# Performance work log

Measured on AMD Instinct MI355X. Metric: run time of the kernel, lower is better.

Reference implementation:

```python
import jax, jax.numpy as jnp
import numpy as np

N_NODES = 1024
HID = 128
NODE_D = 133
BOND_D = 14
E_HALF = 8192  # directed edges; doubled with reverses -> 16384


def setup_inputs() -> dict:
    key = jax.random.key(0)
    ks = jax.random.split(key, 24)

    x = jax.random.normal(ks[0], (N_NODES, NODE_D), jnp.float32)
    edge_attr = jax.random.normal(ks[1], (2 * E_HALF, BOND_D), jnp.float32)
    src = jax.random.randint(ks[2], (E_HALF,), 0, N_NODES)
    dst = jax.random.randint(ks[3], (E_HALF,), 0, N_NODES)
    # bidirectional edges so every edge has a reverse (as _rev_edge_index assumes)
    edge_index = jnp.stack([jnp.concatenate([src, dst]), jnp.concatenate([dst, src])]).astype(jnp.int32)
    rev_edge_index = jnp.concatenate([jnp.arange(E_HALF) + E_HALF, jnp.arange(E_HALF)]).astype(jnp.int32)

    dissociable_masks = (jax.random.uniform(ks[4], (N_NODES,)) < 0.1).astype(jnp.int32)
    pka_raw = jax.random.uniform(ks[5], (N_NODES,), minval=0.0, maxval=14.0)
    valid = jax.random.uniform(ks[6], (N_NODES,)) < (1.0 / 16.0)
    pka_values = jnp.where(valid, pka_raw, jnp.nan).astype(jnp.float32)

    def lin(k, fi, fo):
        return (jax.random.normal(k, (fi, fo)) / np.sqrt(fi)).astype(jnp.float32)

    z = lambda n: jnp.zeros((n,), jnp.float32)
    inp = dict(x=x, edge_attr=edge_attr, pka_values=pka_values,
               dissociable_masks=dissociable_masks, edge_index=edge_index,
               rev_edge_index=rev_edge_index,
               Wi=lin(ks[7], NODE_D + BOND_D, HID), bi=z(HID),
               Wh=lin(ks[8], HID, HID), bh=z(HID),
               Wo=lin(ks[9], NODE_D + HID, HID), bo=z(HID),
               Wnt=lin(ks[10], NODE_D, HID), bnt=z(HID),
               Wc1=lin(ks[11], HID, 256), bc1=z(256),
               Wc2=lin(ks[12], 256, 64), bc2=z(64),
               Wc3=lin(ks[13], 64, 2), bc3=z(2),
               Wr1=lin(ks[14], HID, 256), br1=z(256),
               Wr2=lin(ks[15], 256, 64), br2=z(64),
               Wr3=lin(ks[16], 64, 1), br3=z(1),
               Wg=lin(ks[17], HID, HID), bg=z(HID))
    return inp


def reference(x, edge_attr, pka_values, dissociable_masks, edge_index, rev_edge_index,
              Wi, bi, Wh, bh, Wo, bo, Wnt, bnt,
              Wc1, bc1, Wc2, bc2, Wc3, bc3,
              Wr1, br1, Wr2, br2, Wr3, br3, Wg, bg):
    n = x.shape[0]
    src, dst = edge_index[0], edge_index[1]

    # ---- BondMessagePassing (depth=3, dropout in eval mode) ----
    H0 = jnp.concatenate([x[src], edge_attr], axis=1) @ Wi + bi  # [E, HID]
    Ht = jax.nn.relu(H0)
    for _ in range(2):  # depth - 1 iterations
        agg = jax.ops.segment_sum(Ht, dst, num_segments=n)       # scatter-sum to dst
        M = agg[src] - Ht[rev_edge_index]                        # exclude reverse edge
        Ht = jax.nn.relu(H0 + M @ Wh + bh)
    agg = jax.ops.segment_sum(Ht, dst, num_segments=n)
    tx = x @ Wnt + bnt
    M = jnp.where(jnp.sum(agg, axis=1, keepdims=True) == 0, tx, agg)
    E = jax.nn.relu(jnp.concatenate([x, M], axis=1) @ Wo + bo)   # node embeddings [N, HID]

    valid = ~jnp.isnan(pka_values)
    pka_s = jnp.where(valid, pka_values, 0.0)

    def mlp(e, W1, b1, W2, b2, W3, b3):
        h = jax.nn.relu(e @ W1 + b1)
        h = jax.nn.relu(h @ W2 + b2)
        return h @ W3 + b3

    def step(carry, inp):
        Emb, cls_sum, reg_sum, correct = carry
        i, m_i, p_i, v_i = inp
        e = Emb[i]
        logits = mlp(e, Wc1, bc1, Wc2, bc2, Wc3, bc3)            # [2]
        label = jnp.argmax(logits).astype(jnp.int32)
        target = (m_i > 0).astype(jnp.int32)
        ce = -jax.nn.log_softmax(logits)[target]
        correct = correct + (label == target).astype(jnp.float32)
        reg_cond = (label == 1) | (m_i > 0)
        # sigmoid -> Hardtanh(0,14) (clip is identity on (0,1), kept for fidelity)
        p = jnp.clip(jax.nn.sigmoid(mlp(e, Wr1, br1, Wr2, br2, Wr3, br3))[0], 0.0, 14.0)
        fire = reg_cond & v_i
        reg_sum = reg_sum + jnp.where(fire, (p - p_i) ** 2, 0.0)
        Emb = jax.lax.cond(fire,
                           lambda A: A * (1.0 - jax.nn.sigmoid(A @ Wg + bg)),
                           lambda A: A, Emb)
        return (Emb, cls_sum + ce, reg_sum, correct), (label, jnp.where(reg_cond, p, 0.0))

    init = (E, jnp.float32(0.0), jnp.float32(0.0), jnp.float32(0.0))
    xs = (jnp.arange(n), dissociable_masks, pka_s, valid)
    (_, cls_sum, reg_sum, correct), (labels, preds) = jax.lax.scan(step, init, xs)
    acc = jax.lax.stop_gradient(correct / n)
    loss_vec = jnp.stack([cls_sum + reg_sum, cls_sum, reg_sum, acc])
    return labels, preds, loss_vec
```

## Files before the change

kernel.cpp:

```cpp
#include <hip/hip_runtime.h>

#define NN   1024
#define NE   16384
#define HID  128
#define ND   133
#define BD   14
#define KIN  147
#define NVMAX 128
#define EB   8
#define JF   4
#define JT   2
#define MAXPAIRS (NVMAX * (NVMAX + 1) / 2)
#define TB4 ((MAXPAIRS + JT - 1) / JT)

__device__ __forceinline__ float sigm(float x) { return 1.0f / (1.0f + expf(-x)); }


__global__ void __launch_bounds__(1024)
k_prep3(const int* __restrict__ dst, int* offs, int* elist,
        const float* __restrict__ pka, int* validIdx, int* NvP, int* vpos,
        const int* __restrict__ mask, int* pairCnt, int* pairList,
        int* lossTicket) {
    __shared__ int degS[NN];
    __shared__ int s2[NN];
    __shared__ int fillS[NN];
    __shared__ int elistS[NE];
    __shared__ int vIdxS[NVMAX];
    __shared__ int maskS[NVMAX];
    __shared__ int nvS, pcS;
    int t = threadIdx.x;
    degS[t] = 0;
    float v = pka[t];
    int f = (v == v) ? 1 : 0;
    s2[t] = f;
    __syncthreads();
    for (int e = t; e < NE; e += NN) atomicAdd(&degS[dst[e]], 1);
    __syncthreads();
    int d0 = degS[t];
    __syncthreads();
    for (int st = 1; st < NN; st <<= 1) {
        int a = (t >= st) ? degS[t - st] : 0;
        int b = (t >= st) ? s2[t - st] : 0;
        __syncthreads();
        degS[t] += a; s2[t] += b;
        __syncthreads();
    }
    int hi = degS[t];
    int lo = hi - d0;
    offs[t] = lo;
    fillS[t] = lo;
    if (t == NN - 1) offs[NN] = hi;
    int pos = s2[t] - f;
    int ok = (f && pos < NVMAX) ? 1 : 0;
    vpos[t] = ok ? pos : -1;
    if (ok) { validIdx[pos] = t; vIdxS[pos] = t; }
    if (t == NN - 1) { int nv = (s2[t] > NVMAX) ? NVMAX : s2[t]; *NvP = nv; nvS = nv; }
    if (t == 0) { pcS = 0; *lossTicket = 0; }
    __syncthreads();
    for (int e = t; e < NE; e += NN) { int p = atomicAdd(&fillS[dst[e]], 1); elistS[p] = e; }
    int Nv = nvS;
    if (t < NVMAX) maskS[t] = (t < Nv) ? mask[vIdxS[t]] : 1;
    __syncthreads();
    for (int a = lo + 1; a < hi; a++) {
        int vv = elistS[a]; int b = a - 1;
        while (b >= lo && elistS[b] > vv) { elistS[b + 1] = elistS[b]; b--; }
        elistS[b + 1] = vv;
    }
    for (int idx = t; idx < NVMAX * NVMAX; idx += NN) {
        int vv = idx >> 7, k = idx & (NVMAX - 1);
        if (vv < Nv && k <= vv && maskS[vv] == 0) {
            int p = atomicAdd(&pcS, 1);
            pairList[p] = idx;
        }
    }
    __syncthreads();
    if (t == 0) *pairCnt = pcS;
    for (int e = t; e < NE; e += NN) elist[e] = elistS[e];
}


__global__ void k_edge_init(const float* __restrict__ x, const float* __restrict__ ea,
                            const int* __restrict__ src,
                            const float* __restrict__ Wi, const float* __restrict__ bi,
                            float* __restrict__ H0, float* __restrict__ Ht) {
    __shared__ float in[EB][KIN + 1];
    int e0 = blockIdx.x * EB;
    int h = threadIdx.x;
    for (int j = 0; j < EB; j++) {
        int e = e0 + j; int s = src[e];
        for (int k = h; k < KIN; k += HID)
            in[j][k] = (k < ND) ? x[s * ND + k] : ea[e * BD + (k - ND)];
    }
    __syncthreads();
    float acc[EB];
#pragma unroll
    for (int j = 0; j < EB; j++) acc[j] = 0.f;
    for (int k4 = 0; k4 < KIN / 4; k4++) {
        float w0 = Wi[(4 * k4 + 0) * HID + h];
        float w1 = Wi[(4 * k4 + 1) * HID + h];
        float w2 = Wi[(4 * k4 + 2) * HID + h];
        float w3 = Wi[(4 * k4 + 3) * HID + h];
#pragma unroll
        for (int j = 0; j < EB; j++) {
            const float4 m4 = *(const float4*)&in[j][4 * k4];
            acc[j] = fmaf(m4.x, w0, acc[j]);
            acc[j] = fmaf(m4.y, w1, acc[j]);
            acc[j] = fmaf(m4.z, w2, acc[j]);
            acc[j] = fmaf(m4.w, w3, acc[j]);
        }
    }
    for (int k = (KIN / 4) * 4; k < KIN; k++) {
        float w = Wi[k * HID + h];
#pragma unroll
        for (int j = 0; j < EB; j++) acc[j] = fmaf(in[j][k], w, acc[j]);
    }
    float b = bi[h];
    for (int j = 0; j < EB; j++) {
        float v = acc[j] + b;
        H0[(e0 + j) * HID + h] = v;
        Ht[(e0 + j) * HID + h] = fmaxf(v, 0.f);
    }
}

__global__ void k_segsum(const float* __restrict__ Ht, const int* __restrict__ elist,
                         const int* __restrict__ offs, float* __restrict__ agg) {
    int n = blockIdx.x; int h = threadIdx.x;
    int lo = offs[n], hi = offs[n + 1];
    float a = 0.f;
    for (int j = lo; j < hi; j++) {
        int e = elist[j];
        a += Ht[e * HID + h];
    }
    agg[n * HID + h] = a;
}

__global__ void k_edge_update(const float* __restrict__ H0, const float* __restrict__ Htin,
                              const float* __restrict__ agg,
                              const int* __restrict__ src, const int* __restrict__ rev,
                              const float* __restrict__ Wh, const float* __restrict__ bh,
                              float* __restrict__ Htout) {
    __shared__ float M[EB][HID];
    int e0 = blockIdx.x * EB;
    int h = threadIdx.x;
    for (int j = 0; j < EB; j++) {
        int e = e0 + j; int s = src[e]; int r = rev[e];
        M[j][h] = agg[s * HID + h] - Htin[r * HID + h];
    }
    __syncthreads();
    float acc[EB];
#pragma unroll
    for (int j = 0; j < EB; j++) acc[j] = 0.f;
    for (int k4 = 0; k4 < HID / 4; k4++) {
        float w0 = Wh[(4 * k4 + 0) * HID + h];
        float w1 = Wh[(4 * k4 + 1) * HID + h];
        float w2 = Wh[(4 * k4 + 2) * HID + h];
        float w3 = Wh[(4 * k4 + 3) * HID + h];
#pragma unroll
        for (int j = 0; j < EB; j++) {
            const float4 m4 = *(const float4*)&M[j][4 * k4];
            acc[j] = fmaf(m4.x, w0, acc[j]);
            acc[j] = fmaf(m4.y, w1, acc[j]);
            acc[j] = fmaf(m4.z, w2, acc[j]);
            acc[j] = fmaf(m4.w, w3, acc[j]);
        }
    }
    float b = bh[h];
    for (int j = 0; j < EB; j++) {
        int e = e0 + j;
        Htout[e * HID + h] = fmaxf(H0[e * HID + h] + acc[j] + b, 0.f);
    }
}

__global__ void k_node_embed2(const float* __restrict__ x, const float* __restrict__ Ht,
                              const int* __restrict__ elist, const int* __restrict__ offs,
                              const float* __restrict__ Wnt, const float* __restrict__ bnt,
                              const float* __restrict__ Wo, const float* __restrict__ bo,
                              float* __restrict__ Emb) {
    __shared__ float xs[ND + 1];
    __shared__ float Ms[HID];
    __shared__ float red[HID];
    int n = blockIdx.x; int h = threadIdx.x;
    for (int k = h; k < ND; k += HID) xs[k] = x[n * ND + k];
    int lo = offs[n], hi = offs[n + 1];
    float a = 0.f;
    for (int j = lo; j < hi; j++) a += Ht[elist[j] * HID + h];
    red[h] = a;
    __syncthreads();
    for (int st = 64; st > 0; st >>= 1) { if (h < st) red[h] += red[h + st]; __syncthreads(); }
    float s = red[0];
    __syncthreads();
    float Mh;
    if (s == 0.0f) {
        float t0 = 0.f, t1 = 0.f;
        int k = 0;
        for (; k + 1 < ND; k += 2) {
            t0 = fmaf(xs[k], Wnt[k * HID + h], t0);
            t1 = fmaf(xs[k + 1], Wnt[(k + 1) * HID + h], t1);
        }
        for (; k < ND; k++) t0 = fmaf(xs[k], Wnt[k * HID + h], t0);
        Mh = (t0 + t1) + bnt[h];
    } else {
        Mh = a;
    }
    Ms[h] = Mh;
    __syncthreads();
    float a0 = 0.f, a1 = 0.f;
    int k = 0;
    for (; k + 1 < ND; k += 2) {
        a0 = fmaf(xs[k], Wo[k * HID + h], a0);
        a1 = fmaf(xs[k + 1], Wo[(k + 1) * HID + h], a1);
    }
    for (; k < ND; k++) a0 = fmaf(xs[k], Wo[k * HID + h], a0);
    for (int q = 0; q < HID; q += 2) {
        a0 = fmaf(Ms[q], Wo[(ND + q) * HID + h], a0);
        a1 = fmaf(Ms[q + 1], Wo[(ND + q + 1) * HID + h], a1);
    }
    Emb[n * HID + h] = fmaxf((a0 + a1) + bo[h], 0.f);
}


__global__ void __launch_bounds__(512)
k_chains3(const float* __restrict__ Emb, const int* __restrict__ validIdx,
          const int* __restrict__ NvP,
          const float* __restrict__ Wg, const float* __restrict__ bg,
          float* __restrict__ specSt) {
    int v = blockIdx.x;
    int Nv = *NvP;
    if (v >= Nv) return;
    __shared__ float rS[HID];
    __shared__ float pS[512];
    int tid = threadIdx.x;
    int col = tid & (HID - 1);
    int slot = tid >> 7;
    float wreg[32];
#pragma unroll
    for (int q = 0; q < 32; q++)
        wreg[q] = Wg[(slot * 32 + q) * HID + col];
    float bgc = bg[col];
    int i = validIdx[v];
    if (tid < HID) rS[tid] = Emb[i * HID + tid];
    __syncthreads();
    if (slot == 0) specSt[(size_t)(v * NVMAX + 0) * HID + col] = rS[col];
    int kmax = (v < NVMAX - 1) ? v : (NVMAX - 1);
    for (int k = 1; k <= kmax; k++) {
        const float4* r4 = (const float4*)&rS[slot * 32];
        float px = 0.f, py = 0.f, pz = 0.f, pw = 0.f;
#pragma unroll
        for (int q8 = 0; q8 < 8; q8++) {
            float4 rr = r4[q8];
            px = fmaf(rr.x, wreg[4 * q8 + 0], px);
            py = fmaf(rr.y, wreg[4 * q8 + 1], py);
            pz = fmaf(rr.z, wreg[4 * q8 + 2], pz);
            pw = fmaf(rr.w, wreg[4 * q8 + 3], pw);
        }
        pS[tid] = (px + py) + (pz + pw);
        __syncthreads();
        if (slot == 0) {
            float s = ((pS[col] + pS[col + 128]) + (pS[col + 256] + pS[col + 384])) + bgc;
            float g = 1.0f - sigm(s);
            float nr = rS[col] * g;
            rS[col] = nr;
            specSt[(size_t)(v * NVMAX + k) * HID + col] = nr;
        }
        __syncthreads();
    }
}


__global__ void __launch_bounds__(256)
k_table4(const float* __restrict__ specSt, const int* __restrict__ pairList,
         const int* __restrict__ pairCnt,
         const float* __restrict__ Wc1, const float* __restrict__ bc1,
         const float* __restrict__ Wc2, const float* __restrict__ bc2,
         const float* __restrict__ Wc3, const float* __restrict__ bc3,
         int* __restrict__ labTab) {
    int cnt = *pairCnt;
    int base = blockIdx.x * JT;
    if (base >= cnt) return;
    int nj = cnt - base; if (nj > JT) nj = JT;
    __shared__ float rS[JT][HID];
    __shared__ float h1S[JT][256];
    __shared__ float h2S[JT][64];
    __shared__ int plS[JT];
    int tid = threadIdx.x;
    if (tid < JT) plS[tid] = (tid < nj) ? pairList[base + tid] : 0;
    __syncthreads();
    for (int idx = tid; idx < JT * HID; idx += 256) {
        int j = idx >> 7, k = idx & (HID - 1);
        rS[j][k] = (j < nj) ? specSt[(size_t)plS[j] * HID + k] : 0.f;
    }
    __syncthreads();
    {
        float a[JT];
#pragma unroll
        for (int j = 0; j < JT; j++) a[j] = 0.f;
        for (int k = 0; k < HID; k++) {
            float w = Wc1[k * 256 + tid];
#pragma unroll
            for (int j = 0; j < JT; j++) a[j] = fmaf(rS[j][k], w, a[j]);
        }
        float b1 = bc1[tid];
#pragma unroll
        for (int j = 0; j < JT; j++) h1S[j][tid] = fmaxf(a[j] + b1, 0.f);
    }
    __syncthreads();
    {
        int col = tid & 63, j = tid >> 6;
        if (j < nj) {
            float acc = 0.f;
            for (int k = 0; k < 256; k++)
                acc = fmaf(h1S[j][k], Wc2[k * 64 + col], acc);
            h2S[j][col] = fmaxf(acc + bc2[col], 0.f);
        }
    }
    __syncthreads();
    if (tid < nj) {
        float l0 = bc3[0], l1 = bc3[1];
        for (int k = 0; k < 64; k++) {
            float h = h2S[tid][k];
            l0 = fmaf(h, Wc3[2 * k + 0], l0);
            l1 = fmaf(h, Wc3[2 * k + 1], l1);
        }
        labTab[plS[tid]] = (l1 > l0) ? 1 : 0;
    }
}


__global__ void k_resolve2(const int* __restrict__ validIdx, const int* __restrict__ NvP,
                           const int* __restrict__ mask, const int* __restrict__ labTab,
                           int* fireFlag, int* kPref) {
    __shared__ int vIdxS[NVMAX];
    __shared__ int maskS[NVMAX];
    __shared__ int labS[NVMAX * NVMAX];
    __shared__ int fireS[NN];
    __shared__ int scanS[NN];
    int t = threadIdx.x;
    int Nv = *NvP;
    if (t < NVMAX) {
        int vi = (t < Nv) ? validIdx[t] : 0;
        vIdxS[t] = vi;
        maskS[t] = (t < Nv) ? mask[vi] : 0;
    }
    fireS[t] = 0;
    for (int idx = t; idx < Nv * NVMAX; idx += NN) labS[idx] = labTab[idx];
    __syncthreads();
    if (t == 0) {
        int k = 0;
        for (int v = 0; v < Nv; v++) {
            int fire = (maskS[v] > 0) ? 1 : labS[v * NVMAX + k];
            fireS[vIdxS[v]] = fire;
            k += fire;
        }
    }
    __syncthreads();
    int f0 = fireS[t];
    scanS[t] = f0;
    __syncthreads();
    for (int st = 1; st < NN; st <<= 1) {
        int u = (t >= st) ? scanS[t - st] : 0;
        __syncthreads();
        scanS[t] += u;
        __syncthreads();
    }
    kPref[t] = scanS[t] - f0;
    fireFlag[t] = f0;
}


__global__ void __launch_bounds__(256)
k_final6(const float* __restrict__ Emb, const int* __restrict__ kPref,
         const int* __restrict__ fireFlag, const int* __restrict__ mask,
         const float* __restrict__ pka, const int* __restrict__ vpos,
         const int* __restrict__ labTab,
         const float* __restrict__ Wg, const float* __restrict__ bg,
         const float* __restrict__ Wc1, const float* __restrict__ bc1,
         const float* __restrict__ Wc2, const float* __restrict__ bc2,
         const float* __restrict__ Wc3, const float* __restrict__ bc3,
         const float* __restrict__ Wr1, const float* __restrict__ br1,
         const float* __restrict__ Wr2, const float* __restrict__ br2,
         const float* __restrict__ Wr3, const float* __restrict__ br3,
         float* __restrict__ outLabels, float* __restrict__ outPreds,
         float* __restrict__ ceArr, float* __restrict__ regArr,
         float* __restrict__ corArr, float* __restrict__ outLoss,
         int* __restrict__ lossTicket) {
    __shared__ __align__(16) float WgT[HID * HID];
    __shared__ __align__(16) float rS[JF][HID];
    __shared__ float h1S[JF][256];
    __shared__ float h2S[JF][64];
    __shared__ float lgS[JF][2];
    __shared__ float prS[JF];
    __shared__ int kcS[JF];
    __shared__ int tkS;
    int tid = threadIdx.x;
    int i0 = blockIdx.x * JF;

    {
        char* wbase = (char*)WgT;
        for (int m = 0; m < 64; m++) {
            int idx = tid + m * 256;
            int q = idx >> 7, c = idx & (HID - 1);
            *(float*)(wbase + c * 512 + (((q >> 2) ^ (c & 7)) << 4) + (q & 3) * 4) = Wg[idx];
        }
    }
    if (tid < HID) {
#pragma unroll
        for (int j = 0; j < JF; j++) rS[j][tid] = Emb[(i0 + j) * HID + tid];
    }
    if (tid < JF) kcS[tid] = kPref[i0 + tid];
    __syncthreads();
    int kc[JF]; int maxkc = 0;
#pragma unroll
    for (int j = 0; j < JF; j++) { kc[j] = kcS[j]; if (kc[j] > maxkc) maxkc = kc[j]; }

    int col = tid & (HID - 1);
    int slot = tid >> 7;
    int j0 = slot * 2, j1 = slot * 2 + 1;
    float bgc = bg[col];
    const char* wb = (const char*)WgT + col * 512;
    int cx = col & 7;
    for (int t = 0; t < maxkc; t++) {
        float a00 = 0.f, a01 = 0.f, a02 = 0.f, a03 = 0.f;
        float a10 = 0.f, a11 = 0.f, a12 = 0.f, a13 = 0.f;
        for (int q4 = 0; q4 < 32; q4++) {
            const float4 w4 = *(const float4*)(wb + ((q4 ^ cx) << 4));
            const float4 r0 = *(const float4*)&rS[j0][4 * q4];
            const float4 r1 = *(const float4*)&rS[j1][4 * q4];
            a00 = fmaf(r0.x, w4.x, a00);
            a01 = fmaf(r0.y, w4.y, a01);
            a02 = fmaf(r0.z, w4.z, a02);
            a03 = fmaf(r0.w, w4.w, a03);
            a10 = fmaf(r1.x, w4.x, a10);
            a11 = fmaf(r1.y, w4.y, a11);
            a12 = fmaf(r1.z, w4.z, a12);
            a13 = fmaf(r1.w, w4.w, a13);
        }
        float g0 = 1.0f - sigm(((a00 + a01) + (a02 + a03)) + bgc);
        float g1 = 1.0f - sigm(((a10 + a11) + (a12 + a13)) + bgc);
        __syncthreads();
        if (t < kc[j0]) rS[j0][col] *= g0;
        if (t < kc[j1]) rS[j1][col] *= g1;
        __syncthreads();
    }

    {
        float a[JF];
#pragma unroll
        for (int j = 0; j < JF; j++) a[j] = 0.f;
        for (int k = 0; k < HID; k++) {
            float w = Wc1[k * 256 + tid];
#pragma unroll
            for (int j = 0; j < JF; j++) a[j] = fmaf(rS[j][k], w, a[j]);
        }
        float b = bc1[tid];
#pragma unroll
        for (int j = 0; j < JF; j++) h1S[j][tid] = fmaxf(a[j] + b, 0.f);
    }
    __syncthreads();
    {
        int c2 = tid & 63, j = tid >> 6;
        float acc = 0.f;
        for (int k = 0; k < 256; k++) acc = fmaf(h1S[j][k], Wc2[k * 64 + c2], acc);
        h2S[j][c2] = fmaxf(acc + bc2[c2], 0.f);
    }
    __syncthreads();
    if (tid < 2 * JF) {
        int j = tid >> 1, c = tid & 1;
        float l = bc3[c];
        for (int k = 0; k < 64; k++) l = fmaf(h2S[j][k], Wc3[2 * k + c], l);
        lgS[j][c] = l;
    }
    __syncthreads();

    {
        float a[JF];
#pragma unroll
        for (int j = 0; j < JF; j++) a[j] = 0.f;
        for (int k = 0; k < HID; k++) {
            float w = Wr1[k * 256 + tid];
#pragma unroll
            for (int j = 0; j < JF; j++) a[j] = fmaf(rS[j][k], w, a[j]);
        }
        float b = br1[tid];
#pragma unroll
        for (int j = 0; j < JF; j++) h1S[j][tid] = fmaxf(a[j] + b, 0.f);
    }
    __syncthreads();
    {
        int c2 = tid & 63, j = tid >> 6;
        float acc = 0.f;
        for (int k = 0; k < 256; k++) acc = fmaf(h1S[j][k], Wr2[k * 64 + c2], acc);
        h2S[j][c2] = fmaxf(acc + br2[c2], 0.f);
    }
    __syncthreads();
    if (tid < JF) {
        float pr = br3[0];
        for (int k = 0; k < 64; k++) pr = fmaf(h2S[tid][k], Wr3[k], pr);
        prS[tid] = pr;
    }
    __syncthreads();

    if (tid < JF) {
        int j = tid, i = i0 + j;
        float l0 = lgS[j][0], l1 = lgS[j][1];
        int compLab = (l1 > l0) ? 1 : 0;
        int vp = vpos[i];
        int label = (vp >= 0 && mask[i] == 0) ? labTab[vp * NVMAX + kc[j]] : compLab;
        int target = (mask[i] > 0) ? 1 : 0;
        float mx = fmaxf(l0, l1);
        float lse = mx + logf(expf(l0 - mx) + expf(l1 - mx));
        float ce = lse - ((target == 1) ? l1 : l0);
        int reg_cond = (label == 1) || (mask[i] > 0);
        float p = sigm(prS[j]);
        p = fminf(fmaxf(p, 0.f), 14.f);
        outLabels[i] = (float)label;
        outPreds[i] = reg_cond ? p : 0.f;
        ceArr[i] = ce;
        corArr[i] = (label == target) ? 1.f : 0.f;
        if (fireFlag[i]) {
            float d = p - pka[i];
            regArr[i] = d * d;
        } else {
            regArr[i] = 0.f;
        }
    }

    __threadfence();
    __syncthreads();
    if (tid == 0) tkS = atomicAdd(lossTicket, 1);
    __syncthreads();
    if (tkS == (NN / JF) - 1) {
        __threadfence();
        __shared__ float s[256];
        float a = ((ceArr[tid] + ceArr[tid + 256]) + (ceArr[tid + 512] + ceArr[tid + 768]));
        s[tid] = a; __syncthreads();
        for (int st = 128; st > 0; st >>= 1) { if (tid < st) s[tid] += s[tid + st]; __syncthreads(); }
        float cls = s[0]; __syncthreads();
        a = ((regArr[tid] + regArr[tid + 256]) + (regArr[tid + 512] + regArr[tid + 768]));
        s[tid] = a; __syncthreads();
        for (int st = 128; st > 0; st >>= 1) { if (tid < st) s[tid] += s[tid + st]; __syncthreads(); }
        float reg = s[0]; __syncthreads();
        a = ((corArr[tid] + corArr[tid + 256]) + (corArr[tid + 512] + corArr[tid + 768]));
        s[tid] = a; __syncthreads();
        for (int st = 128; st > 0; st >>= 1) { if (tid < st) s[tid] += s[tid + st]; __syncthreads(); }
        float cor = s[0];
        if (tid == 0) {
            outLoss[0] = cls + reg;
            outLoss[1] = cls;
            outLoss[2] = reg;
            outLoss[3] = cor / (float)NN;
        }
    }
}


extern "C" void kernel_launch(void* const* d_in, const int* in_sizes, int n_in,
                              void* d_out, int out_size, void* d_ws, size_t ws_size,
                              hipStream_t stream) {
    const float* x    = (const float*)d_in[0];
    const float* ea   = (const float*)d_in[1];
    const float* pka  = (const float*)d_in[2];
    const int*   mask = (const int*)d_in[3];
    const int*   eidx = (const int*)d_in[4];
    const int*   rev  = (const int*)d_in[5];
    const float* Wi  = (const float*)d_in[6];  const float* bi  = (const float*)d_in[7];
    const float* Wh  = (const float*)d_in[8];  const float* bh  = (const float*)d_in[9];
    const float* Wo  = (const float*)d_in[10]; const float* bo  = (const float*)d_in[11];
    const float* Wnt = (const float*)d_in[12]; const float* bnt = (const float*)d_in[13];
    const float* Wc1 = (const float*)d_in[14]; const float* bc1 = (const float*)d_in[15];
    const float* Wc2 = (const float*)d_in[16]; const float* bc2 = (const float*)d_in[17];
    const float* Wc3 = (const float*)d_in[18]; const float* bc3 = (const float*)d_in[19];
    const float* Wr1 = (const float*)d_in[20]; const float* br1 = (const float*)d_in[21];
    const float* Wr2 = (const float*)d_in[22]; const float* br2 = (const float*)d_in[23];
    const float* Wr3 = (const float*)d_in[24]; const float* br3 = (const float*)d_in[25];
    const float* Wg  = (const float*)d_in[26]; const float* bg  = (const float*)d_in[27];

    const int* src = eidx;
    const int* dst = eidx + NE;

    char* w = (char*)d_ws;
    auto alloc = [&](size_t bytes) -> void* {
        void* p = (void*)w;
        w += ((bytes + 255) / 256) * 256;
        return p;
    };
    float* H0   = (float*)alloc((size_t)NE * HID * 4);
    float* HtA  = (float*)alloc((size_t)NE * HID * 4);
    float* HtB  = (float*)alloc((size_t)NE * HID * 4);
    float* agg  = (float*)alloc((size_t)NN * HID * 4);
    float* Emb  = (float*)alloc((size_t)NN * HID * 4);
    int* offs    = (int*)alloc((NN + 1) * 4);
    int* elist   = (int*)alloc(NE * 4);
    int* validIdx= (int*)alloc(NVMAX * 4);
    int* NvP     = (int*)alloc(16);
    int* vpos    = (int*)alloc(NN * 4);
    int* fireFlag= (int*)alloc(NN * 4);
    int* kPref   = (int*)alloc(NN * 4);
    float* specSt= (float*)alloc((size_t)NVMAX * NVMAX * HID * 4);
    int* labTab  = (int*)alloc(NVMAX * NVMAX * 4);
    int* pairCnt = (int*)alloc(16);
    int* pairList= (int*)alloc(MAXPAIRS * 4);
    int* lossTicket = (int*)alloc(16);
    float* ceArr = (float*)alloc(NN * 4);
    float* regArr= (float*)alloc(NN * 4);
    float* corArr= (float*)alloc(NN * 4);

    float* outF = (float*)d_out;

    k_prep3<<<1, NN, 0, stream>>>(dst, offs, elist, pka, validIdx, NvP, vpos,
                                  mask, pairCnt, pairList, lossTicket);

    k_edge_init<<<NE / EB, HID, 0, stream>>>(x, ea, src, Wi, bi, H0, HtA);
    k_segsum<<<NN, HID, 0, stream>>>(HtA, elist, offs, agg);
    k_edge_update<<<NE / EB, HID, 0, stream>>>(H0, HtA, agg, src, rev, Wh, bh, HtB);
    k_segsum<<<NN, HID, 0, stream>>>(HtB, elist, offs, agg);
    k_edge_update<<<NE / EB, HID, 0, stream>>>(H0, HtB, agg, src, rev, Wh, bh, HtA);
    k_node_embed2<<<NN, HID, 0, stream>>>(x, HtA, elist, offs, Wnt, bnt, Wo, bo, Emb);

    k_chains3<<<NVMAX, 512, 0, stream>>>(Emb, validIdx, NvP, Wg, bg, specSt);
    k_table4<<<TB4, 256, 0, stream>>>(specSt, pairList, pairCnt,
                                      Wc1, bc1, Wc2, bc2, Wc3, bc3, labTab);
    k_resolve2<<<1, NN, 0, stream>>>(validIdx, NvP, mask, labTab, fireFlag, kPref);

    k_final6<<<NN / JF, 256, 0, stream>>>(Emb, kPref, fireFlag, mask, pka, vpos, labTab,
                                          Wg, bg, Wc1, bc1, Wc2, bc2, Wc3, bc3,
                                          Wr1, br1, Wr2, br2, Wr3, br3,
                                          outF, outF + NN, ceArr, regArr, corArr,
                                          outF + 2 * NN, lossTicket);
}
```

Before: 216.7 us.

## Restructure gating matvec in final kernel as split-K with register tiling

The repeated Wg gating matvec in the final kernel now partitions work by output column group and K-slice. Each thread computes a 4-column by 4-row register tile over 16 K values, and partial sums are reduced through a new shared buffer. The Wg copy into shared memory becomes a plain float4 copy without the swizzle. This cuts shared-memory reads per FMA and raises instruction-level parallelism, at the cost of an extra reduction pass, an extra barrier per step and 16KB more shared memory per block.

```diff
diff --git a/kernel.cpp b/kernel.cpp
--- a/kernel.cpp
+++ b/kernel.cpp
@@ -368,7 +368,7 @@
 
 
 __global__ void __launch_bounds__(256)
-k_final6(const float* __restrict__ Emb, const int* __restrict__ kPref,
+k_final8(const float* __restrict__ Emb, const int* __restrict__ kPref,
          const int* __restrict__ fireFlag, const int* __restrict__ mask,
          const float* __restrict__ pka, const int* __restrict__ vpos,
          const int* __restrict__ labTab,
@@ -383,8 +383,9 @@
          float* __restrict__ ceArr, float* __restrict__ regArr,
          float* __restrict__ corArr, float* __restrict__ outLoss,
          int* __restrict__ lossTicket) {
-    __shared__ __align__(16) float WgT[HID * HID];
+    __shared__ __align__(16) float WgS[HID * HID];
     __shared__ __align__(16) float rS[JF][HID];
+    __shared__ __align__(16) float pS[JF][8][HID];
     __shared__ float h1S[JF][256];
     __shared__ float h2S[JF][64];
     __shared__ float lgS[JF][2];
@@ -394,14 +395,9 @@
     int tid = threadIdx.x;
     int i0 = blockIdx.x * JF;
 
-    {
-        char* wbase = (char*)WgT;
-        for (int m = 0; m < 64; m++) {
-            int idx = tid + m * 256;
-            int q = idx >> 7, c = idx & (HID - 1);
-            *(float*)(wbase + c * 512 + (((q >> 2) ^ (c & 7)) << 4) + (q & 3) * 4) = Wg[idx];
-        }
-    }
+    const float4* Wg4 = (const float4*)Wg;
+    float4* Ws4 = (float4*)WgS;
+    for (int idx = tid; idx < HID * HID / 4; idx += 256) Ws4[idx] = Wg4[idx];
     if (tid < HID) {
 #pragma unroll
         for (int j = 0; j < JF; j++) rS[j][tid] = Emb[(i0 + j) * HID + tid];
@@ -412,33 +408,68 @@
 #pragma unroll
     for (int j = 0; j < JF; j++) { kc[j] = kcS[j]; if (kc[j] > maxkc) maxkc = kc[j]; }
 
-    int col = tid & (HID - 1);
-    int slot = tid >> 7;
-    int j0 = slot * 2, j1 = slot * 2 + 1;
-    float bgc = bg[col];
-    const char* wb = (const char*)WgT + col * 512;
-    int cx = col & 7;
+    int cg = tid & 31;
+    int qs = tid >> 5;
+    int q0 = qs * 16;
+    int rc = tid & (HID - 1);
+    int rh = tid >> 7;
+    float bgc = bg[rc];
+    const float4* WgS4 = (const float4*)WgS;
     for (int t = 0; t < maxkc; t++) {
-        float a00 = 0.f, a01 = 0.f, a02 = 0.f, a03 = 0.f;
-        float a10 = 0.f, a11 = 0.f, a12 = 0.f, a13 = 0.f;
-        for (int q4 = 0; q4 < 32; q4++) {
-            const float4 w4 = *(const float4*)(wb + ((q4 ^ cx) << 4));
-            const float4 r0 = *(const float4*)&rS[j0][4 * q4];
-            const float4 r1 = *(const float4*)&rS[j1][4 * q4];
-            a00 = fmaf(r0.x, w4.x, a00);
-            a01 = fmaf(r0.y, w4.y, a01);
-            a02 = fmaf(r0.z, w4.z, a02);
-            a03 = fmaf(r0.w, w4.w, a03);
-            a10 = fmaf(r1.x, w4.x, a10);
-            a11 = fmaf(r1.y, w4.y, a11);
-            a12 = fmaf(r1.z, w4.z, a12);
-            a13 = fmaf(r1.w, w4.w, a13);
-        }
-        float g0 = 1.0f - sigm(((a00 + a01) + (a02 + a03)) + bgc);
-        float g1 = 1.0f - sigm(((a10 + a11) + (a12 + a13)) + bgc);
-        __syncthreads();
-        if (t < kc[j0]) rS[j0][col] *= g0;
-        if (t < kc[j1]) rS[j1][col] *= g1;
+        float4 acc[JF];
+#pragma unroll
+        for (int j = 0; j < JF; j++) acc[j] = make_float4(0.f, 0.f, 0.f, 0.f);
+        for (int qq = 0; qq < 16; qq += 4) {
+            int q = q0 + qq;
+            const float4 w0 = WgS4[(q + 0) * 32 + cg];
+            const float4 w1 = WgS4[(q + 1) * 32 + cg];
+            const float4 w2 = WgS4[(q + 2) * 32 + cg];
+            const float4 w3 = WgS4[(q + 3) * 32 + cg];
+#pragma unroll
+            for (int j = 0; j < JF; j++) {
+                const float4 r = *(const float4*)&rS[j][q];
+                acc[j].x = fmaf(r.x, w0.x, acc[j].x);
+                acc[j].x = fmaf(r.y, w1.x, acc[j].x);
+                acc[j].x = fmaf(r.z, w2.x, acc[j].x);
+                acc[j].x = fmaf(r.w, w3.x, acc[j].x);
+                acc[j].y = fmaf(r.x, w0.y, acc[j].y);
+                acc[j].y = fmaf(r.y, w1.y, acc[j].y);
+                acc[j].y = fmaf(r.z, w2.y, acc[j].y);
+                acc[j].y = fmaf(r.w, w3.y, acc[j].y);
+                acc[j].z = fmaf(r.x, w0.z, acc[j].z);
+                acc[j].z = fmaf(r.y, w1.z, acc[j].z);
+                acc[j].z = fmaf(r.z, w2.z, acc[j].z);
+                acc[j].z = fmaf(r.w, w3.z, acc[j].z);
+                acc[j].w = fmaf(r.x, w0.w, acc[j].w);
+                acc[j].w = fmaf(r.y, w1.w, acc[j].w);
+                acc[j].w = fmaf(r.z, w2.w, acc[j].w);
+                acc[j].w = fmaf(r.w, w3.w, acc[j].w);
+            }
+        }
+#pragma unroll
+        for (int j = 0; j < JF; j++)
+            *(float4*)&pS[j][qs][4 * cg] = acc[j];
+        __syncthreads();
+        float nr0, nr1;
+        {
+            int j = 2 * rh;
+            float s = pS[j][0][rc];
+#pragma unroll
+            for (int z = 1; z < 8; z++) s += pS[j][z][rc];
+            float g = 1.0f - sigm(s + bgc);
+            nr0 = (t < kc[j]) ? rS[j][rc] * g : rS[j][rc];
+        }
+        {
+            int j = 2 * rh + 1;
+            float s = pS[j][0][rc];
+#pragma unroll
+            for (int z = 1; z < 8; z++) s += pS[j][z][rc];
+            float g = 1.0f - sigm(s + bgc);
+            nr1 = (t < kc[j]) ? rS[j][rc] * g : rS[j][rc];
+        }
+        __syncthreads();
+        rS[2 * rh][rc] = nr0;
+        rS[2 * rh + 1][rc] = nr1;
         __syncthreads();
     }
 
@@ -621,7 +652,7 @@
                                       Wc1, bc1, Wc2, bc2, Wc3, bc3, labTab);
     k_resolve2<<<1, NN, 0, stream>>>(validIdx, NvP, mask, labTab, fireFlag, kPref);
 
-    k_final6<<<NN / JF, 256, 0, stream>>>(Emb, kPref, fireFlag, mask, pka, vpos, labTab,
+    k_final8<<<NN / JF, 256, 0, stream>>>(Emb, kPref, fireFlag, mask, pka, vpos, labTab,
                                           Wg, bg, Wc1, bc1, Wc2, bc2, Wc3, bc3,
                                           Wr1, br1, Wr2, br2, Wr3, br3,
                                           outF, outF + NN, ceArr, regArr, corArr,
```

Result: no change. 215.5 us, median of 2 (-0.6%).
